# Kernel optimization log

Hardware: AMD Instinct MI355X
Metric: run time of the kernel (lower is better)

The kernel has to match this reference:

```python
import jax, jax.numpy as jnp
import numpy as np

B, S, D, H = 4, 2048, 1024, 16
HD = D // H  # head dim = 64


def setup_inputs() -> dict:
    key = jax.random.key(0)
    ks = jax.random.split(key, 7)
    sc = 0.02
    return {
        "x": jax.random.normal(ks[0], (B, S, D), dtype=jnp.float32),
        "Wq": jax.random.normal(ks[1], (D, D), dtype=jnp.float32) * sc,
        "bq": jax.random.normal(ks[2], (D,), dtype=jnp.float32) * sc,
        "Wk": jax.random.normal(ks[3], (D, D), dtype=jnp.float32) * sc,
        "bk": jax.random.normal(ks[4], (D,), dtype=jnp.float32) * sc,
        "Wv": jax.random.normal(ks[5], (D, D), dtype=jnp.float32) * sc,
        "bv": jax.random.normal(ks[6], (D,), dtype=jnp.float32) * sc,
    }


def reference(x, Wq, bq, Wk, bk, Wv, bv):
    # Linear projections (torch Linear: x @ W.T + b); W here stored as [out, in]
    def split_heads(t):  # [B,S,D] -> [B,H,S,HD]
        return t.reshape(B, S, H, HD).transpose(0, 2, 1, 3)

    q = split_heads(jnp.einsum('bsd,ed->bse', x, Wq) + bq)
    k = split_heads(jnp.einsum('bsd,ed->bse', x, Wk) + bk)
    v = split_heads(jnp.einsum('bsd,ed->bse', x, Wv) + bv)

    # NOTE: original applies no 1/sqrt(head_dim) scaling
    scores = jnp.einsum('bhqd,bhkd->bhqk', q, k)        # [B,H,S,S]
    probs = jax.nn.softmax(scores, axis=-1)             # dropout = identity (eval)
    ctx = jnp.einsum('bhqk,bhkd->bhqd', probs, v)       # [B,H,S,HD]
    out = ctx.transpose(0, 2, 1, 3).reshape(B, S, D)    # [B,S,D]
    return out, probs
```

## Files before the change

### kernel.cpp

```cpp
#include <hip/hip_runtime.h>
#include <hip/hip_bf16.h>

typedef unsigned short u16;
typedef unsigned int   u32;

constexpr int B = 4, S = 2048, D = 1024, H = 16, HD = 64;
constexpr int M = B * S;
constexpr size_t TEN = (size_t)M * D;

using bf16x8 = __attribute__((ext_vector_type(8))) short;
using f32x4  = __attribute__((ext_vector_type(4))) float;

__device__ __forceinline__ u16 f2bf(float f) {
    u32 u = __float_as_uint(f);
    u += 0x7fffu + ((u >> 16) & 1u);
    return (u16)(u >> 16);
}
__device__ __forceinline__ u32 pack2(u16 a, u16 b) { return (u32)a | ((u32)b << 16); }

__device__ __forceinline__ void gll16(const u16* gsrc, u16* ldst) {
    __builtin_amdgcn_global_load_lds(
        (const __attribute__((address_space(1))) u32*)gsrc,
        (__attribute__((address_space(3))) u32*)ldst,
        16, 0, 0);
}

constexpr size_t NX8 = TEN / 8;
constexpr size_t NW8 = (size_t)D * D / 8;

__global__ __launch_bounds__(256) void convert_kernel(
    const float* __restrict__ x,
    const float* __restrict__ Wq, const float* __restrict__ Wk,
    const float* __restrict__ Wv,
    u16* __restrict__ xbf, u16* __restrict__ wbf)
{
    size_t i = (size_t)blockIdx.x * 256 + threadIdx.x;
    if (i < NX8) {
        float4 f0 = *((const float4*)x + i * 2);
        float4 f1 = *((const float4*)x + i * 2 + 1);
        float f[8] = {f0.x, f0.y, f0.z, f0.w, f1.x, f1.y, f1.z, f1.w};
        u16 h[8];
        #pragma unroll
        for (int e = 0; e < 8; ++e) h[e] = f2bf(f[e]);
        *(uint4*)(xbf + i * 8) = make_uint4(pack2(h[0],h[1]), pack2(h[2],h[3]),
                                            pack2(h[4],h[5]), pack2(h[6],h[7]));
    } else if (i < NX8 + 3 * NW8) {
        size_t j = i - NX8;
        const float* Wsrc;
        size_t jj;
        if (j < NW8)            { Wsrc = Wq; jj = j; }
        else if (j < 2 * NW8)   { Wsrc = Wk; jj = j - NW8; }
        else                    { Wsrc = Wv; jj = j - 2 * NW8; }
        float4 f0 = *((const float4*)Wsrc + jj * 2);
        float4 f1 = *((const float4*)Wsrc + jj * 2 + 1);
        float f[8] = {f0.x, f0.y, f0.z, f0.w, f1.x, f1.y, f1.z, f1.w};
        u16 h[8];
        #pragma unroll
        for (int e = 0; e < 8; ++e) h[e] = f2bf(f[e]);
        *(uint4*)(wbf + j * 8) = make_uint4(pack2(h[0],h[1]), pack2(h[2],h[3]),
                                            pack2(h[4],h[5]), pack2(h[6],h[7]));
    }
}

constexpr int GBM = 128, GBN = 128, GBK = 32;
constexpr int NKT = D / GBK;

__global__ __launch_bounds__(256, 3) void qkv_proj_kernel(
    const u16* __restrict__ xbf, const u16* __restrict__ wbf,
    const float* __restrict__ bq, const float* __restrict__ bk,
    const float* __restrict__ bv,
    u16* __restrict__ wsq, u16* __restrict__ wsk, u16* __restrict__ wvt)
{
    const int lin    = blockIdx.x;
    const int xcd    = lin & 7;
    const int local  = lin >> 3;
    const int wg     = local >> 3;
    const int zi     = wg >> 3;
    const int ny     = wg & 7;
    const int mstrip = xcd * 8 + (local & 7);

    const u16* __restrict__ Wz = wbf + (size_t)zi * D * D;
    const float* __restrict__ bias = (zi == 0) ? bq : (zi == 1) ? bk : bv;

    const int m0 = mstrip * GBM;
    const int n0 = ny * GBN;
    const int h0 = n0 >> 6;
    const int tid = threadIdx.x;
    const int w = tid >> 6, lane = tid & 63;
    const int l15 = lane & 15, lg = lane >> 4;

    __shared__ __align__(16) u16 Ah[2][GBM * GBK];
    __shared__ __align__(16) u16 Bt[2][GBN * GBK];

    const u16* __restrict__ xb_b = xbf + (size_t)m0 * D;
    const u16* __restrict__ wz_b = Wz + (size_t)n0 * D;

    f32x4 acc[2][8];
    #pragma unroll
    for (int mi = 0; mi < 2; ++mi)
        #pragma unroll
        for (int ni = 0; ni < 8; ++ni) acc[mi][ni] = (f32x4){0.f,0.f,0.f,0.f};

    auto stage = [&](int kt, int bb) {
        const int kofs = kt * GBK;
        #pragma unroll
        for (int p = 0; p < 2; ++p) {
            int c = w * 128 + p * 64 + lane;
            int r = c >> 2, s = c & 3;
            int sc = (s ^ (r & 3)) * 8;
            const size_t go = (size_t)r * D + kofs + sc;
            gll16(xb_b + go, &Ah[bb][(w * 128 + p * 64) * 8]);
            gll16(wz_b + go, &Bt[bb][(w * 128 + p * 64) * 8]);
        }
    };

    stage(0, 0);
    __syncthreads();

    for (int kt = 0; kt < NKT; ++kt) {
        const int cur = kt & 1;
        if (kt < NKT - 1) stage(kt + 1, cur ^ 1);

        #pragma unroll
        for (int half = 0; half < 2; ++half) {
            bf16x8 bfr[4];
            #pragma unroll
            for (int ni4 = 0; ni4 < 4; ++ni4) {
                int brow = (half * 4 + ni4) * 16 + l15;
                bfr[ni4] = *(const bf16x8*)&Bt[cur][brow * GBK + ((lg ^ (brow & 3)) * 8)];
            }
            #pragma unroll
            for (int mi = 0; mi < 2; ++mi) {
                int arow = w * 32 + mi * 16 + l15;
                int so = (lg ^ (arow & 3)) * 8;
                bf16x8 ah = *(const bf16x8*)&Ah[cur][arow * GBK + so];
                #pragma unroll
                for (int ni4 = 0; ni4 < 4; ++ni4)
                    acc[mi][half * 4 + ni4] = __builtin_amdgcn_mfma_f32_16x16x32_bf16(
                        ah, bfr[ni4], acc[mi][half * 4 + ni4], 0, 0, 0);
            }
        }
        __syncthreads();
    }

    float bv8[8];
    #pragma unroll
    for (int ni = 0; ni < 8; ++ni) bv8[ni] = bias[n0 + ni * 16 + l15];

    if (zi < 2) {
        u16* __restrict__ dst = (zi == 0) ? wsq : wsk;
        #pragma unroll
        for (int mi = 0; mi < 2; ++mi) {
            #pragma unroll
            for (int r = 0; r < 4; ++r) {
                int m = m0 + w * 32 + mi * 16 + lg * 4 + r;
                int bb = m >> 11, s = m & 2047;
                #pragma unroll
                for (int ni = 0; ni < 8; ++ni) {
                    int h = h0 + (ni >> 2);
                    int hd = (ni & 3) * 16 + l15;
                    dst[((size_t)(bb * H + h) * S + s) * HD + hd] =
                        f2bf(acc[mi][ni][r] + bv8[ni]);
                }
            }
        }
    } else {
        #pragma unroll
        for (int mi = 0; mi < 2; ++mi) {
            int mb = m0 + w * 32 + mi * 16 + lg * 4;
            int bb = mb >> 11, s0 = mb & 2047;
            #pragma unroll
            for (int ni = 0; ni < 8; ++ni) {
                int h = h0 + (ni >> 2);
                int hd = (ni & 3) * 16 + l15;
                u16 e0 = f2bf(acc[mi][ni][0] + bv8[ni]);
                u16 e1 = f2bf(acc[mi][ni][1] + bv8[ni]);
                u16 e2 = f2bf(acc[mi][ni][2] + bv8[ni]);
                u16 e3 = f2bf(acc[mi][ni][3] + bv8[ni]);
                *(uint2*)(wvt + ((size_t)(bb * H + h) * HD + hd) * S + s0) =
                    make_uint2(pack2(e0, e1), pack2(e2, e3));
            }
        }
    }
}

__global__ __launch_bounds__(1024) void attn_fused_kernel(
    const u16* __restrict__ qg, const u16* __restrict__ kg,
    const u16* __restrict__ vtg, float* __restrict__ probs,
    float* __restrict__ out)
{
    const int lin = blockIdx.x;
    const int swz = (lin & 7) * 64 + (lin >> 3);
    const int bh = swz >> 3;
    const int m0 = (swz & 7) * 256;

    const int b = bh >> 4, h = bh & 15;
    const int tid = threadIdx.x;
    const int w = tid >> 6, lane = tid & 63;
    const int l15 = lane & 15, lg = lane >> 4;

    const u16* __restrict__ qb  = qg  + (size_t)bh * S * HD;
    const u16* __restrict__ kbp = kg  + (size_t)bh * S * HD;
    const u16* __restrict__ vtb = vtg + (size_t)bh * HD * S;
    float* __restrict__ pb = probs + ((size_t)bh * S + m0) * (size_t)S;

    __shared__ __align__(16) u16 Ks[2][64 * 64];
    __shared__ __align__(16) u16 Vts[2][64 * 64];
    __shared__ __align__(16) u16 Pl[16][16 * 64];

    bf16x8 aq[2];
    {
        const u16* qr = qb + (size_t)(m0 + w * 16 + l15) * HD + lg * 8;
        aq[0] = *(const bf16x8*)(qr);
        aq[1] = *(const bf16x8*)(qr + 32);
    }

    auto stageK = [&](int t, int bb) {
        if (w < 8) {
            int c = w * 64 + lane;
            int r = c >> 3, s = c & 7;
            int sc = (s ^ (r & 7)) * 8;
            gll16(kbp + (size_t)(t * 64 + r) * 64 + sc, &Ks[bb][(w * 64) * 8]);
        }
    };
    auto stageV = [&](int t, int bb) {
        if (w >= 8) {
            int c = (w - 8) * 64 + lane;
            int r = c >> 3, s = c & 7;
            int sc = (s ^ (r & 7)) * 8;
            gll16(vtb + (size_t)r * S + t * 64 + sc, &Vts[bb][((w - 8) * 64) * 8]);
        }
    };

    float lacc = 0.f;
    stageK(0, 0);
    __syncthreads();

    for (int t = 0; t < 32; ++t) {
        const int cur = t & 1;
        if (t < 31) stageK(t + 1, cur ^ 1);
        f32x4 acc[4];
        #pragma unroll
        for (int n = 0; n < 4; ++n) acc[n] = (f32x4){0.f, 0.f, 0.f, 0.f};
        __builtin_amdgcn_s_setprio(1);
        #pragma unroll
        for (int n = 0; n < 4; ++n) {
            #pragma unroll
            for (int kk = 0; kk < 2; ++kk) {
                int row = n * 16 + l15;
                int sl = (kk * 4 + lg) ^ (row & 7);
                bf16x8 bk_ = *(const bf16x8*)&Ks[cur][row * 64 + sl * 8];
                acc[n] = __builtin_amdgcn_mfma_f32_16x16x32_bf16(bk_, aq[kk], acc[n], 0, 0, 0);
            }
        }
        __builtin_amdgcn_s_setprio(0);
        #pragma unroll
        for (int n = 0; n < 4; ++n)
            #pragma unroll
            for (int r = 0; r < 4; ++r)
                lacc += __expf(acc[n][r]);
        __syncthreads();
    }

    lacc += __shfl_xor(lacc, 16, 64);
    lacc += __shfl_xor(lacc, 32, 64);
    const float inv_l = 1.f / lacc;

    f32x4 accO[4];
    #pragma unroll
    for (int n = 0; n < 4; ++n) accO[n] = (f32x4){0.f, 0.f, 0.f, 0.f};

    stageK(0, 0);
    stageV(0, 0);
    __syncthreads();

    float* pqrow = pb + (size_t)(w * 16 + l15) * S + lg * 4;

    for (int t = 0; t < 32; ++t) {
        const int cur = t & 1;
        if (t < 31) { stageK(t + 1, cur ^ 1); stageV(t + 1, cur ^ 1); }

        f32x4 acc[4];
        #pragma unroll
        for (int n = 0; n < 4; ++n) acc[n] = (f32x4){0.f, 0.f, 0.f, 0.f};
        __builtin_amdgcn_s_setprio(1);
        #pragma unroll
        for (int n = 0; n < 4; ++n) {
            #pragma unroll
            for (int kk = 0; kk < 2; ++kk) {
                int row = n * 16 + l15;
                int sl = (kk * 4 + lg) ^ (row & 7);
                bf16x8 bk_ = *(const bf16x8*)&Ks[cur][row * 64 + sl * 8];
                acc[n] = __builtin_amdgcn_mfma_f32_16x16x32_bf16(bk_, aq[kk], acc[n], 0, 0, 0);
            }
        }
        __builtin_amdgcn_s_setprio(0);

        #pragma unroll
        for (int n = 0; n < 4; ++n) {
            float e0 = __expf(acc[n][0]) * inv_l;
            float e1 = __expf(acc[n][1]) * inv_l;
            float e2 = __expf(acc[n][2]) * inv_l;
            float e3 = __expf(acc[n][3]) * inv_l;
            f32x4 p4 = (f32x4){e0, e1, e2, e3};
            __builtin_nontemporal_store(p4, (f32x4*)(pqrow + t * 64 + n * 16));
            uint2 pk2 = make_uint2(pack2(f2bf(e0), f2bf(e1)),
                                   pack2(f2bf(e2), f2bf(e3)));
            int s16 = (2 * n + (lg >> 1)) ^ (l15 & 7);
            *(uint2*)&Pl[w][l15 * 64 + s16 * 8 + (lg & 1) * 4] = pk2;
        }

        bf16x8 af[2];
        #pragma unroll
        for (int kk2 = 0; kk2 < 2; ++kk2) {
            int s16 = (kk2 * 4 + lg) ^ (l15 & 7);
            af[kk2] = *(const bf16x8*)&Pl[w][l15 * 64 + s16 * 8];
        }

        __builtin_amdgcn_s_setprio(1);
        #pragma unroll
        for (int n = 0; n < 4; ++n) {
            #pragma unroll
            for (int kk2 = 0; kk2 < 2; ++kk2) {
                int row = n * 16 + l15;
                int sl = (kk2 * 4 + lg) ^ (row & 7);
                bf16x8 bv = *(const bf16x8*)&Vts[cur][row * 64 + sl * 8];
                accO[n] = __builtin_amdgcn_mfma_f32_16x16x32_bf16(af[kk2], bv, accO[n], 0, 0, 0);
            }
        }
        __builtin_amdgcn_s_setprio(0);
        __syncthreads();
    }

    #pragma unroll
    for (int n = 0; n < 4; ++n)
        #pragma unroll
        for (int r = 0; r < 4; ++r)
            out[((size_t)b * S + m0 + w * 16 + lg * 4 + r) * D + h * HD + n * 16 + l15] =
                accO[n][r];
}

extern "C" void kernel_launch(void* const* d_in, const int* in_sizes, int n_in,
                              void* d_out, int out_size, void* d_ws, size_t ws_size,
                              hipStream_t stream)
{
    const float* x  = (const float*)d_in[0];
    const float* Wq = (const float*)d_in[1];
    const float* bq = (const float*)d_in[2];
    const float* Wk = (const float*)d_in[3];
    const float* bk = (const float*)d_in[4];
    const float* Wv = (const float*)d_in[5];
    const float* bv = (const float*)d_in[6];

    float* out   = (float*)d_out;
    float* probs = out + (size_t)B * S * D;

    u16* wsq = (u16*)d_ws;
    u16* wsk = wsq + TEN;
    u16* wvt = wsk + TEN;
    u16* xbf = wvt + TEN;
    u16* wbf = xbf + TEN;
    (void)ws_size;

    dim3 gc((unsigned)((NX8 + 3 * NW8 + 255) / 256));
    convert_kernel<<<gc, 256, 0, stream>>>(x, Wq, Wk, Wv, xbf, wbf);

    qkv_proj_kernel<<<dim3(1536), 256, 0, stream>>>(xbf, wbf, bq, bk, bv,
                                                    wsq, wsk, wvt);

    attn_fused_kernel<<<dim3(512), 1024, 0, stream>>>(wsq, wsk, wvt, probs, out);
}
```

Baseline: 421.2 us.

## Triple-buffer K/V staging with explicit vmcnt waits instead of __syncthreads

Grows the LDS K and V staging buffers from two to three and prefetches two tiles ahead in both attention passes. The full __syncthreads at the end of each iteration is replaced by a raw s_barrier preceded by a partial s_waitcnt vmcnt, so waves wait only for the load they need next. In the second pass this avoids draining the nontemporal probability stores every iteration. The risk is correctness: the hand-counted vmcnt values depend on in-order completion of loads and stores and on the exact number of stores per iteration. It also uses more LDS.

Measured after the change: 419.6 us (median of 2 runs). Within noise of the previous version (-0.4%).

```diff
diff --git a/kernel.cpp b/kernel.cpp
--- a/kernel.cpp
+++ b/kernel.cpp
@@ -204,8 +204,8 @@
     const u16* __restrict__ vtb = vtg + (size_t)bh * HD * S;
     float* __restrict__ pb = probs + ((size_t)bh * S + m0) * (size_t)S;
 
-    __shared__ __align__(16) u16 Ks[2][64 * 64];
-    __shared__ __align__(16) u16 Vts[2][64 * 64];
+    __shared__ __align__(16) u16 Ks[3][64 * 64];
+    __shared__ __align__(16) u16 Vts[3][64 * 64];
     __shared__ __align__(16) u16 Pl[16][16 * 64];
 
     bf16x8 aq[2];
@@ -234,32 +234,42 @@
 
     float lacc = 0.f;
     stageK(0, 0);
-    __syncthreads();
-
-    for (int t = 0; t < 32; ++t) {
-        const int cur = t & 1;
-        if (t < 31) stageK(t + 1, cur ^ 1);
-        f32x4 acc[4];
-        #pragma unroll
-        for (int n = 0; n < 4; ++n) acc[n] = (f32x4){0.f, 0.f, 0.f, 0.f};
-        __builtin_amdgcn_s_setprio(1);
-        #pragma unroll
-        for (int n = 0; n < 4; ++n) {
-            #pragma unroll
-            for (int kk = 0; kk < 2; ++kk) {
-                int row = n * 16 + l15;
-                int sl = (kk * 4 + lg) ^ (row & 7);
-                bf16x8 bk_ = *(const bf16x8*)&Ks[cur][row * 64 + sl * 8];
-                acc[n] = __builtin_amdgcn_mfma_f32_16x16x32_bf16(bk_, aq[kk], acc[n], 0, 0, 0);
-            }
-        }
-        __builtin_amdgcn_s_setprio(0);
-        #pragma unroll
-        for (int n = 0; n < 4; ++n)
-            #pragma unroll
-            for (int r = 0; r < 4; ++r)
-                lacc += __expf(acc[n][r]);
-        __syncthreads();
+    stageK(1, 1);
+    asm volatile("s_waitcnt vmcnt(1)" ::: "memory");
+    __builtin_amdgcn_s_barrier();
+    __builtin_amdgcn_sched_barrier(0);
+
+    {
+        int cur = 0, stg = 2;
+        for (int t = 0; t < 32; ++t) {
+            if (t < 30) stageK(t + 2, stg);
+            f32x4 acc[4];
+            #pragma unroll
+            for (int n = 0; n < 4; ++n) acc[n] = (f32x4){0.f, 0.f, 0.f, 0.f};
+            __builtin_amdgcn_s_setprio(1);
+            #pragma unroll
+            for (int n = 0; n < 4; ++n) {
+                #pragma unroll
+                for (int kk = 0; kk < 2; ++kk) {
+                    int row = n * 16 + l15;
+                    int sl = (kk * 4 + lg) ^ (row & 7);
+                    bf16x8 bk_ = *(const bf16x8*)&Ks[cur][row * 64 + sl * 8];
+                    acc[n] = __builtin_amdgcn_mfma_f32_16x16x32_bf16(bk_, aq[kk], acc[n], 0, 0, 0);
+                }
+            }
+            __builtin_amdgcn_s_setprio(0);
+            #pragma unroll
+            for (int n = 0; n < 4; ++n)
+                #pragma unroll
+                for (int r = 0; r < 4; ++r)
+                    lacc += __expf(acc[n][r]);
+            if (t < 30)      asm volatile("s_waitcnt vmcnt(1)" ::: "memory");
+            else if (t == 30) asm volatile("s_waitcnt vmcnt(0)" ::: "memory");
+            __builtin_amdgcn_s_barrier();
+            __builtin_amdgcn_sched_barrier(0);
+            cur = (cur == 2) ? 0 : cur + 1;
+            stg = (stg == 2) ? 0 : stg + 1;
+        }
     }
 
     lacc += __shfl_xor(lacc, 16, 64);
@@ -270,66 +280,76 @@
     #pragma unroll
     for (int n = 0; n < 4; ++n) accO[n] = (f32x4){0.f, 0.f, 0.f, 0.f};
 
-    stageK(0, 0);
-    stageV(0, 0);
-    __syncthreads();
+    stageK(0, 0); stageV(0, 0);
+    stageK(1, 1); stageV(1, 1);
+    asm volatile("s_waitcnt vmcnt(1)" ::: "memory");
+    __builtin_amdgcn_s_barrier();
+    __builtin_amdgcn_sched_barrier(0);
 
     float* pqrow = pb + (size_t)(w * 16 + l15) * S + lg * 4;
 
-    for (int t = 0; t < 32; ++t) {
-        const int cur = t & 1;
-        if (t < 31) { stageK(t + 1, cur ^ 1); stageV(t + 1, cur ^ 1); }
-
-        f32x4 acc[4];
-        #pragma unroll
-        for (int n = 0; n < 4; ++n) acc[n] = (f32x4){0.f, 0.f, 0.f, 0.f};
-        __builtin_amdgcn_s_setprio(1);
-        #pragma unroll
-        for (int n = 0; n < 4; ++n) {
-            #pragma unroll
-            for (int kk = 0; kk < 2; ++kk) {
-                int row = n * 16 + l15;
-                int sl = (kk * 4 + lg) ^ (row & 7);
-                bf16x8 bk_ = *(const bf16x8*)&Ks[cur][row * 64 + sl * 8];
-                acc[n] = __builtin_amdgcn_mfma_f32_16x16x32_bf16(bk_, aq[kk], acc[n], 0, 0, 0);
-            }
-        }
-        __builtin_amdgcn_s_setprio(0);
-
-        #pragma unroll
-        for (int n = 0; n < 4; ++n) {
-            float e0 = __expf(acc[n][0]) * inv_l;
-            float e1 = __expf(acc[n][1]) * inv_l;
-            float e2 = __expf(acc[n][2]) * inv_l;
-            float e3 = __expf(acc[n][3]) * inv_l;
-            f32x4 p4 = (f32x4){e0, e1, e2, e3};
-            __builtin_nontemporal_store(p4, (f32x4*)(pqrow + t * 64 + n * 16));
-            uint2 pk2 = make_uint2(pack2(f2bf(e0), f2bf(e1)),
-                                   pack2(f2bf(e2), f2bf(e3)));
-            int s16 = (2 * n + (lg >> 1)) ^ (l15 & 7);
-            *(uint2*)&Pl[w][l15 * 64 + s16 * 8 + (lg & 1) * 4] = pk2;
-        }
-
-        bf16x8 af[2];
-        #pragma unroll
-        for (int kk2 = 0; kk2 < 2; ++kk2) {
-            int s16 = (kk2 * 4 + lg) ^ (l15 & 7);
-            af[kk2] = *(const bf16x8*)&Pl[w][l15 * 64 + s16 * 8];
-        }
-
-        __builtin_amdgcn_s_setprio(1);
-        #pragma unroll
-        for (int n = 0; n < 4; ++n) {
+    {
+        int cur = 0, stg = 2;
+        for (int t = 0; t < 32; ++t) {
+            if (t < 30) { stageK(t + 2, stg); stageV(t + 2, stg); }
+
+            f32x4 acc[4];
+            #pragma unroll
+            for (int n = 0; n < 4; ++n) acc[n] = (f32x4){0.f, 0.f, 0.f, 0.f};
+            __builtin_amdgcn_s_setprio(1);
+            #pragma unroll
+            for (int n = 0; n < 4; ++n) {
+                #pragma unroll
+                for (int kk = 0; kk < 2; ++kk) {
+                    int row = n * 16 + l15;
+                    int sl = (kk * 4 + lg) ^ (row & 7);
+                    bf16x8 bk_ = *(const bf16x8*)&Ks[cur][row * 64 + sl * 8];
+                    acc[n] = __builtin_amdgcn_mfma_f32_16x16x32_bf16(bk_, aq[kk], acc[n], 0, 0, 0);
+                }
+            }
+            __builtin_amdgcn_s_setprio(0);
+
+            #pragma unroll
+            for (int n = 0; n < 4; ++n) {
+                float e0 = __expf(acc[n][0]) * inv_l;
+                float e1 = __expf(acc[n][1]) * inv_l;
+                float e2 = __expf(acc[n][2]) * inv_l;
+                float e3 = __expf(acc[n][3]) * inv_l;
+                f32x4 p4 = (f32x4){e0, e1, e2, e3};
+                __builtin_nontemporal_store(p4, (f32x4*)(pqrow + t * 64 + n * 16));
+                uint2 pk2 = make_uint2(pack2(f2bf(e0), f2bf(e1)),
+                                       pack2(f2bf(e2), f2bf(e3)));
+                int s16 = (2 * n + (lg >> 1)) ^ (l15 & 7);
+                *(uint2*)&Pl[w][l15 * 64 + s16 * 8 + (lg & 1) * 4] = pk2;
+            }
+
+            bf16x8 af[2];
             #pragma unroll
             for (int kk2 = 0; kk2 < 2; ++kk2) {
-                int row = n * 16 + l15;
-                int sl = (kk2 * 4 + lg) ^ (row & 7);
-                bf16x8 bv = *(const bf16x8*)&Vts[cur][row * 64 + sl * 8];
-                accO[n] = __builtin_amdgcn_mfma_f32_16x16x32_bf16(af[kk2], bv, accO[n], 0, 0, 0);
-            }
-        }
-        __builtin_amdgcn_s_setprio(0);
-        __syncthreads();
+                int s16 = (kk2 * 4 + lg) ^ (l15 & 7);
+                af[kk2] = *(const bf16x8*)&Pl[w][l15 * 64 + s16 * 8];
+            }
+
+            __builtin_amdgcn_s_setprio(1);
+            #pragma unroll
+            for (int n = 0; n < 4; ++n) {
+                #pragma unroll
+                for (int kk2 = 0; kk2 < 2; ++kk2) {
+                    int row = n * 16 + l15;
+                    int sl = (kk2 * 4 + lg) ^ (row & 7);
+                    bf16x8 bv = *(const bf16x8*)&Vts[cur][row * 64 + sl * 8];
+                    accO[n] = __builtin_amdgcn_mfma_f32_16x16x32_bf16(af[kk2], bv, accO[n], 0, 0, 0);
+                }
+            }
+            __builtin_amdgcn_s_setprio(0);
+
+            if (t < 30)      asm volatile("s_waitcnt vmcnt(5)" ::: "memory");
+            else if (t == 30) asm volatile("s_waitcnt vmcnt(4)" ::: "memory");
+            __builtin_amdgcn_s_barrier();
+            __builtin_amdgcn_sched_barrier(0);
+            cur = (cur == 2) ? 0 : cur + 1;
+            stg = (stg == 2) ? 0 : stg + 1;
+        }
     }
 
     #pragma unroll
```
